# Kernel optimization log

Measured on AMD Instinct MI355X. Metric: run time of the kernel, lower is better.

The kernel has to match this reference:

```python
import jax, jax.numpy as jnp
import numpy as np

STRIDES = (8, 16, 32)
NC = 80            # num_classes
BINS = 16          # dfl_bins
TOPK = 10          # tal_topk
TAL_ALPHA, TAL_BETA = 0.5, 6.0   # ultralytics TaskAlignedAssigner defaults
EPS = 1e-9
FOCAL_A, FOCAL_G = 0.25, 2.0
W_CLS, W_IOU, W_DFL = 0.5, 7.5, 1.5


def _make_grid(H, W, stride):
    ys, xs = jnp.meshgrid(jnp.arange(H, dtype=jnp.float32), jnp.arange(W, dtype=jnp.float32), indexing='ij')
    return jnp.stack([(xs + 0.5) * stride, (ys + 0.5) * stride], -1).reshape(H * W, 2)


def _flatten(p):
    # (B,C,H,W) -> cls (B,N,NC), dfl (B,N,4,BINS); channel layout = [4*BINS dfl | NC cls]
    B, C, H, W = p.shape
    p = p.transpose(0, 2, 3, 1).reshape(B, H * W, C)
    return p[..., 4 * BINS:], p[..., :4 * BINS].reshape(B, H * W, 4, BINS)


def _pairwise_iou(gt, pr):
    # gt (B,G,4), pr (B,N,4) -> iou (B,G,N)
    g = gt[:, :, None]
    p = pr[:, None]
    lt = jnp.maximum(g[..., :2], p[..., :2])
    rb = jnp.minimum(g[..., 2:], p[..., 2:])
    wh = jnp.clip(rb - lt, 0.0)
    inter = wh[..., 0] * wh[..., 1]
    ag = (g[..., 2] - g[..., 0]) * (g[..., 3] - g[..., 1])
    ap = jnp.clip(p[..., 2] - p[..., 0], 0.0) * jnp.clip(p[..., 3] - p[..., 1], 0.0)
    return inter / (ag + ap - inter + EPS)


def _ciou_loss(p, t):
    # elementwise CIoU loss, (...,4) xyxy -> (...)
    px1, py1, px2, py2 = p[..., 0], p[..., 1], p[..., 2], p[..., 3]
    tx1, ty1, tx2, ty2 = t[..., 0], t[..., 1], t[..., 2], t[..., 3]
    w1, h1 = px2 - px1, py2 - py1
    w2, h2 = tx2 - tx1, ty2 - ty1
    inter = jnp.clip(jnp.minimum(px2, tx2) - jnp.maximum(px1, tx1), 0.0) * \
            jnp.clip(jnp.minimum(py2, ty2) - jnp.maximum(py1, ty1), 0.0)
    union = w1 * h1 + w2 * h2 - inter + EPS
    iou = inter / union
    cw = jnp.maximum(px2, tx2) - jnp.minimum(px1, tx1)
    ch = jnp.maximum(py2, ty2) - jnp.minimum(py1, ty1)
    c2 = cw * cw + ch * ch + EPS
    rho2 = ((px1 + px2 - tx1 - tx2) ** 2 + (py1 + py2 - ty1 - ty2) ** 2) / 4.0
    v = (4.0 / np.pi ** 2) * (jnp.arctan(w2 / (h2 + EPS)) - jnp.arctan(w1 / (h1 + EPS))) ** 2
    alpha = jax.lax.stop_gradient(v / (v - iou + (1.0 + EPS)))
    return 1.0 - (iou - rho2 / c2 - v * alpha)


def _tal_assign(cls_prob, pred_boxes, grids, gt_bboxes, gt_labels):
    B, N, C = cls_prob.shape
    G = gt_bboxes.shape[1]
    idx = jnp.broadcast_to(gt_labels[:, None, :], (B, N, G))
    scores = jnp.take_along_axis(cls_prob, idx, axis=2).transpose(0, 2, 1)  # (B,G,N)
    overlaps = _pairwise_iou(gt_bboxes, pred_boxes)                          # (B,G,N)
    align = scores ** TAL_ALPHA * overlaps ** TAL_BETA
    x, y = grids[:, 0], grids[:, 1]
    in_gts = ((x[None, None] > gt_bboxes[..., 0:1]) & (x[None, None] < gt_bboxes[..., 2:3]) &
              (y[None, None] > gt_bboxes[..., 1:2]) & (y[None, None] < gt_bboxes[..., 3:4]))
    metric = jnp.where(in_gts, align, 0.0)
    vals, idxs = jax.lax.top_k(metric, TOPK)                                 # (B,G,TOPK)
    bi = jnp.arange(B)[:, None, None]
    gi = jnp.arange(G)[None, :, None]
    topk_mask = jnp.zeros((B, G, N), bool).at[bi, gi, idxs].set(vals > EPS)
    mask_pos = topk_mask & in_gts
    multi = mask_pos.sum(1) > 1                                              # (B,N)
    is_max = jnp.argmax(overlaps, 1)[:, None, :] == jnp.arange(G)[None, :, None]
    mask_pos = jnp.where(multi[:, None, :], is_max, mask_pos)
    fg = mask_pos.any(1)                                                     # (B,N)
    matched = jnp.argmax(mask_pos, 1)                                        # (B,N)
    mi = jnp.where(fg, matched, -1)
    b2 = jnp.arange(B)[:, None]
    tb = gt_bboxes[b2, matched]                                              # (B,N,4)
    tl = gt_labels[b2, matched]                                              # (B,N)
    mpf = mask_pos.astype(align.dtype)
    align_m = align * mpf
    ov_m = overlaps * mpf
    norm = (align_m * ov_m.max(-1, keepdims=True) / (align_m.max(-1, keepdims=True) + EPS)).max(1)
    ts = jax.nn.one_hot(tl, C, dtype=align.dtype) * norm[..., None] * fg[..., None]
    return ts, tb, fg, mi


def _dfl_targets(gt_bboxes, mi, fgf, grids, stride_map):
    # vectorized version of _make_dfl_targets: soft two-bin scatter per coord
    B, N = mi.shape
    b2 = jnp.arange(B)[:, None]
    boxes = gt_bboxes[b2, jnp.maximum(mi, 0)]                                # (B,N,4)
    cx, cy = grids[:, 0], grids[:, 1]
    d = jnp.stack([jnp.clip(cx - boxes[..., 0], 0.0), jnp.clip(cy - boxes[..., 1], 0.0),
                   jnp.clip(boxes[..., 2] - cx, 0.0), jnp.clip(boxes[..., 3] - cy, 0.0)], -1)
    d = jnp.clip(d / stride_map[None, :, None], 0.0, BINS - 1 - 1e-6)
    lo = jnp.floor(d)
    a = d - lo
    lo_i = lo.astype(jnp.int32)
    up_i = jnp.minimum(lo_i + 1, BINS - 1)
    td = jax.nn.one_hot(lo_i, BINS) * (1.0 - a)[..., None] + jax.nn.one_hot(up_i, BINS) * a[..., None]
    return td * fgf[..., None, None]                                         # (B,N,4,BINS)


def _focal_sum(logits, targets):
    logits = logits.reshape(-1, NC)
    targets = targets.reshape(-1, NC)
    p = jax.nn.sigmoid(logits)
    # stable BCE-with-logits
    ce = jnp.maximum(logits, 0.0) - logits * targets + jnp.log1p(jnp.exp(-jnp.abs(logits)))
    p_t = p * targets + (1.0 - p) * (1.0 - targets)
    a_t = targets * FOCAL_A + (1.0 - targets) * (1.0 - FOCAL_A)
    return (a_t * (1.0 - p_t) ** FOCAL_G * ce).sum()


def _loss(p0, p1, p2, gt_bboxes, gt_labels):
    cls_l, dfl_l, grid_l, str_l = [], [], [], []
    for p, s in zip((p0, p1, p2), STRIDES):
        c, d = _flatten(p)
        cls_l.append(c)
        dfl_l.append(d)
        H, W = p.shape[2], p.shape[3]
        grid_l.append(_make_grid(H, W, s))
        str_l.append(jnp.full((H * W,), float(s), jnp.float32))
    all_cls = jnp.concatenate(cls_l, 1)       # (B,N,NC)
    all_dfl = jnp.concatenate(dfl_l, 1)       # (B,N,4,BINS)
    grids = jnp.concatenate(grid_l, 0)        # (N,2)
    stride_map = jnp.concatenate(str_l, 0)    # (N,)
    # DFL decode: expectation over bins * stride -> ltrb -> xyxy
    dist = (jax.nn.softmax(all_dfl, -1) * jnp.arange(BINS, dtype=jnp.float32)).sum(-1) * stride_map[None, :, None]
    cx, cy = grids[:, 0], grids[:, 1]
    pred_boxes = jnp.stack([cx - dist[..., 0], cy - dist[..., 1], cx + dist[..., 2], cy + dist[..., 3]], -1)
    # assignment under stop_gradient (torch.no_grad in the original)
    cls_prob = jax.lax.stop_gradient(jax.nn.sigmoid(all_cls))
    pb_sg = jax.lax.stop_gradient(pred_boxes)
    ts, tb, fg, mi = _tal_assign(cls_prob, pb_sg, grids, gt_bboxes, gt_labels)
    ts = jax.lax.stop_gradient(ts)
    tb = jax.lax.stop_gradient(tb)
    fgf = fg.astype(jnp.float32)
    den = jnp.maximum(fg.sum(), 1).astype(jnp.float32)
    loss_iou = (_ciou_loss(pred_boxes, tb) * fgf).sum() / den
    tdfl = _dfl_targets(gt_bboxes, mi, fgf, grids, stride_map)
    loss_dfl = -(tdfl * jax.nn.log_softmax(all_dfl, -1)).sum() / den
    loss_cls = _focal_sum(all_cls, ts) / den
    return jnp.stack([W_IOU * loss_iou, W_DFL * loss_dfl, W_CLS * loss_cls])


def setup_inputs() -> dict:
    key = jax.random.key(0)
    ks = jax.random.split(key, 5)
    B, G = 16, 32
    p0 = jax.random.normal(ks[0], (B, 4 * BINS + NC, 80, 80), jnp.float32)
    p1 = jax.random.normal(ks[1], (B, 4 * BINS + NC, 40, 40), jnp.float32)
    p2 = jax.random.normal(ks[2], (B, 4 * BINS + NC, 20, 20), jnp.float32)
    u = jax.random.uniform(ks[3], (B, G, 4), jnp.float32)
    x1 = u[..., 0] * 560.0
    y1 = u[..., 1] * 560.0
    w = u[..., 2] * 140.0 + 20.0
    h = u[..., 3] * 140.0 + 20.0
    gt_bboxes = jnp.stack([x1, y1, jnp.minimum(x1 + w, 640.0), jnp.minimum(y1 + h, 640.0)], -1)
    gt_labels = jax.random.randint(ks[4], (B, G), 0, NC, jnp.int32)
    return {"p0": p0, "p1": p1, "p2": p2, "gt_bboxes": gt_bboxes, "gt_labels": gt_labels}


def reference(p0, p1, p2, gt_bboxes, gt_labels):
    return _loss(p0, p1, p2, gt_bboxes, gt_labels)
```

## Files before the change

### kernel.cpp

```cpp
#include <hip/hip_runtime.h>
#include <hip/hip_bf16.h>
#include <math.h>

#define NCC 80
#define BINS 16
#define NCH 144
#define NB 16
#define NG 32
#define NA 8400
#define HW0 6400
#define HW1 1600
#define HW2 400
#define TOPKK 10
#define EPSF 1e-9f
#define MAXE 13
#define MAXFG (NB*NG*TOPKK)
#define NMASK (NB*NA)
#define FOCAL_BLOCKS 2625

__device__ __forceinline__ void anchor_geom(int n, float& cx, float& cy, float& st){
    if(n < HW0){ int y=n/80, x=n-y*80; st=8.f; cx=(x+0.5f)*8.f; cy=(y+0.5f)*8.f; }
    else if(n < HW0+HW1){ int m=n-HW0; int y=m/40, x=m-y*40; st=16.f; cx=(x+0.5f)*16.f; cy=(y+0.5f)*16.f; }
    else { int m=n-(HW0+HW1); int y=m/20, x=m-y*20; st=32.f; cx=(x+0.5f)*32.f; cy=(y+0.5f)*32.f; }
}

__device__ __forceinline__ const float* level_base(const float* p0, const float* p1, const float* p2,
                                                   int b, int n, int& m, int& hw){
    if(n < HW0){ m=n; hw=HW0; return p0 + (size_t)b*NCH*HW0; }
    if(n < HW0+HW1){ m=n-HW0; hw=HW1; return p1 + (size_t)b*NCH*HW1; }
    m=n-(HW0+HW1); hw=HW2; return p2 + (size_t)b*NCH*HW2;
}

__device__ __forceinline__ float iou_gp(float gx1,float gy1,float gx2,float gy2,
                                        float px1,float py1,float px2,float py2){
    float ltx = fmaxf(gx1, px1), lty = fmaxf(gy1, py1);
    float rbx = fminf(gx2, px2), rby = fminf(gy2, py2);
    float w = fmaxf(rbx-ltx, 0.f), h = fmaxf(rby-lty, 0.f);
    float inter = w*h;
    float ag = (gx2-gx1)*(gy2-gy1);
    float ap = fmaxf(px2-px1,0.f)*fmaxf(py2-py1,0.f);
    return inter/(ag+ap-inter+EPSF);
}

__device__ __forceinline__ float focal0(float x, float& p, float& ce0){
    float ax = fabsf(x);
    float e  = __expf(-ax);
    float r  = 1.f/(1.f+e);
    p   = (x >= 0.f) ? r : 1.f - r;
    ce0 = fmaxf(x,0.f) + __logf(1.f+e);
    return 0.75f*p*p*ce0;
}

__global__ __launch_bounds__(256) void k_decode(const float* __restrict__ p0, const float* __restrict__ p1,
                                                const float* __restrict__ p2, float* __restrict__ boxc,
                                                unsigned* __restrict__ maskg, float* __restrict__ amax,
                                                float* __restrict__ omax, int* __restrict__ cnt){
    int l = blockIdx.x*256 + threadIdx.x;
    if(l < NMASK) maskg[l] = 0u;
    if(l < NB*NG){ amax[l] = 0.f; omax[l] = 0.f; }
    if(l == 0) *cnt = 0;
    int n = l % NA;
    int j = (l / NA) & 3;
    int b = l / (NA*4);
    int m, hw; const float* base = level_base(p0,p1,p2,b,n,m,hw);
    float cx, cy, st; anchor_geom(n,cx,cy,st);
    const float* ch = base + (size_t)(j*BINS)*hw + m;
    float v[BINS]; float mx=-1e30f;
    #pragma unroll
    for(int k=0;k<BINS;k++){ v[k]=ch[(size_t)k*hw]; mx = fmaxf(mx, v[k]); }
    float s=0.f, acc=0.f;
    #pragma unroll
    for(int k=0;k<BINS;k++){ float e=__expf(v[k]-mx); s+=e; acc+=e*(float)k; }
    float d = acc/s*st;
    float out;
    if(j==0) out = cx - d;
    else if(j==1) out = cy - d;
    else if(j==2) out = cx + d;
    else out = cy + d;
    boxc[(size_t)j*NB*NA + (size_t)b*NA + n] = out;
}

__global__ __launch_bounds__(256) void k_assign(const float* __restrict__ p0, const float* __restrict__ p1,
                                                const float* __restrict__ p2, const float* __restrict__ boxc,
                                                const float* __restrict__ gtb, const int* __restrict__ gtl,
                                                unsigned* __restrict__ maskg){
    int wv = threadIdx.x >> 6, lane = threadIdx.x & 63;
    int g = blockIdx.x*4 + wv, b = blockIdx.y;
    const float* gb = gtb + ((size_t)b*NG + g)*4;
    float gx1=gb[0], gy1=gb[1], gx2=gb[2], gy2=gb[3];
    int label = gtl[b*NG+g];
    const float* bx1 = boxc + (size_t)b*NA;
    const float* by1 = bx1 + (size_t)NB*NA;
    const float* bx2 = by1 + (size_t)NB*NA;
    const float* by2 = bx2 + (size_t)NB*NA;

    int xs[3], ys[3], nx[3], cc[3];
    #pragma unroll
    for(int lvl=0; lvl<3; lvl++){
        float s = (float)(8<<lvl); int D = 80>>lvl;
        int x0 = max(0, (int)floorf(gx1/s - 0.5f));
        int x1 = min(D-1, (int)ceilf (gx2/s - 0.5f));
        int y0 = max(0, (int)floorf(gy1/s - 0.5f));
        int y1 = min(D-1, (int)ceilf (gy2/s - 0.5f));
        xs[lvl]=x0; ys[lvl]=y0;
        nx[lvl]=max(0, x1-x0+1);
        int nyv=max(0, y1-y0+1);
        cc[lvl]=nx[lvl]*nyv;
    }
    int t0 = cc[0], t01 = cc[0]+cc[1], total = t01+cc[2];

    float mv[MAXE]; int mn[MAXE];
    #pragma unroll
    for(int j=0;j<MAXE;j++){
        int ci = lane + 64*j;
        float met = -1.f; int n = 0x7fffffff;
        if(ci < total){
            int lvl, rel;
            if(ci < t0){ lvl=0; rel=ci; }
            else if(ci < t01){ lvl=1; rel=ci-t0; }
            else { lvl=2; rel=ci-t01; }
            int yy = ys[lvl] + rel / nx[lvl];
            int xx = xs[lvl] + rel % nx[lvl];
            int D = 80>>lvl; float s = (float)(8<<lvl);
            int off = (lvl==0)?0:((lvl==1)?HW0:(HW0+HW1));
            n = off + yy*D + xx;
            float cx = (xx+0.5f)*s, cy = (yy+0.5f)*s;
            met = 0.f;
            if((cx>gx1)&&(cx<gx2)&&(cy>gy1)&&(cy<gy2)){
                float ov = iou_gp(gx1,gy1,gx2,gy2, bx1[n],by1[n],bx2[n],by2[n]);
                int m,hw; const float* base = level_base(p0,p1,p2,b,n,m,hw);
                float x = base[(size_t)(4*BINS+label)*hw + m];
                float sg = 1.f/(1.f+__expf(-x));
                float ov2 = ov*ov;
                met = sqrtf(sg)*(ov2*ov2*ov2);
            }
        }
        mv[j]=met; mn[j]=n;
    }

    for(int k=0;k<TOPKK;k++){
        float bv = -1.f; int bi = 0x7fffffff;
        #pragma unroll
        for(int j=0;j<MAXE;j++){
            if(mv[j] > bv || (mv[j] == bv && mn[j] < bi)){ bv=mv[j]; bi=mn[j]; }
        }
        #pragma unroll
        for(int off=1; off<64; off<<=1){
            float ov = __shfl_xor(bv, off);
            int   oi = __shfl_xor(bi, off);
            if(ov > bv || (ov == bv && oi < bi)){ bv=ov; bi=oi; }
        }
        if(bv <= EPSF) break;
        bool own = false;
        #pragma unroll
        for(int j=0;j<MAXE;j++){
            if(mn[j] == bi && mv[j] > -1.f){ mv[j] = -1.f; own = true; }
        }
        if(own) atomicOr(&maskg[(size_t)b*NA + bi], 1u<<g);
    }
}

__global__ __launch_bounds__(256) void k_resolve(const float* __restrict__ p0, const float* __restrict__ p1,
                                                 const float* __restrict__ p2, const float* __restrict__ boxc,
                                                 const float* __restrict__ gtb, const int* __restrict__ gtl,
                                                 const unsigned* __restrict__ maskg,
                                                 float* __restrict__ amax, float* __restrict__ omax,
                                                 int* __restrict__ cnt, unsigned* __restrict__ fglist,
                                                 float* __restrict__ fgalign, float* __restrict__ fgx){
    __shared__ float sgt[NG*4];
    __shared__ int wcnt[4];
    __shared__ int sbase;
    int tid = threadIdx.x; int b = blockIdx.y;
    int wv = tid >> 6, lane = tid & 63;
    if(tid < NG*4) sgt[tid] = gtb[(size_t)b*NG*4 + tid];
    __syncthreads();
    int n = blockIdx.x*256 + tid;
    size_t bn = (size_t)b*NA + n;
    unsigned mask = (n < NA) ? maskg[bn] : 0u;
    bool fg = (mask != 0u);

    int match = 0; float ov = 0.f, av = 0.f, x = 0.f;
    if(fg){
        float px1 = boxc[bn], py1 = boxc[(size_t)NB*NA+bn],
              px2 = boxc[2*(size_t)NB*NA+bn], py2 = boxc[3*(size_t)NB*NA+bn];
        if(__popc(mask) > 1){
            float best = -1.f; int bi = 0;
            for(int g=0; g<NG; g++){
                float o = iou_gp(sgt[g*4],sgt[g*4+1],sgt[g*4+2],sgt[g*4+3],px1,py1,px2,py2);
                if(o > best){ best=o; bi=g; }
            }
            match = bi; ov = best;
        } else {
            match = __ffs(mask)-1;
            ov = iou_gp(sgt[match*4],sgt[match*4+1],sgt[match*4+2],sgt[match*4+3],px1,py1,px2,py2);
        }
        int label = gtl[b*NG+match];
        int m,hw; const float* base = level_base(p0,p1,p2,b,n,m,hw);
        x = base[(size_t)(4*BINS+label)*hw + m];
        float sg = 1.f/(1.f+__expf(-x));
        float ov2 = ov*ov;
        av = sqrtf(sg)*(ov2*ov2*ov2);
        atomicMax((int*)&amax[b*NG+match], __float_as_int(av));
        atomicMax((int*)&omax[b*NG+match], __float_as_int(ov));
    }
    unsigned long long bal = __ballot(fg);
    if(lane==0) wcnt[wv] = __popcll(bal);
    __syncthreads();
    if(tid==0){
        int tot = wcnt[0]+wcnt[1]+wcnt[2]+wcnt[3];
        sbase = tot ? atomicAdd(cnt, tot) : 0;
    }
    __syncthreads();
    if(fg){
        int woff = 0;
        for(int w=0; w<wv; w++) woff += wcnt[w];
        int before = __popcll(bal & ((1ull<<lane)-1ull));
        int pos = sbase + woff + before;
        fglist[pos]  = (unsigned)bn | ((unsigned)match << 18);
        fgalign[pos] = av;
        fgx[pos]     = x;
    }
}

__global__ __launch_bounds__(256) void k_fg(const float* __restrict__ p0, const float* __restrict__ p1,
                                            const float* __restrict__ p2, const float* __restrict__ boxc,
                                            const float* __restrict__ gtb, const int* __restrict__ gtl,
                                            const float* __restrict__ amax, const float* __restrict__ omax,
                                            const int* __restrict__ cnt, const unsigned* __restrict__ fglist,
                                            const float* __restrict__ fgalign, const float* __restrict__ fgx,
                                            float* __restrict__ piou, float* __restrict__ pdfl,
                                            float* __restrict__ pfix){
    __shared__ float s4[12];
    int tid = threadIdx.x;
    int i = blockIdx.x*256 + tid;
    float iou_l = 0.f, dfl_l = 0.f, fix_l = 0.f;
    if(i < *cnt){
        unsigned e = fglist[i];
        int bn = e & 0x3FFFF;
        int g  = e >> 18;
        int b  = bn / NA;
        int n  = bn - b*NA;
        float align = fgalign[i];
        float norm = align * omax[b*NG+g] / (amax[b*NG+g] + EPSF);

        const float* gb = gtb + ((size_t)b*NG+g)*4;
        float tx1=gb[0], ty1=gb[1], tx2=gb[2], ty2=gb[3];
        float px1 = boxc[bn], py1 = boxc[(size_t)NB*NA+bn],
              px2 = boxc[2*(size_t)NB*NA+bn], py2 = boxc[3*(size_t)NB*NA+bn];
        float w1=px2-px1, h1=py2-py1, w2=tx2-tx1, h2=ty2-ty1;
        float inter = fmaxf(fminf(px2,tx2)-fmaxf(px1,tx1),0.f) *
                      fmaxf(fminf(py2,ty2)-fmaxf(py1,ty1),0.f);
        float uni = w1*h1 + w2*h2 - inter + EPSF;
        float iou = inter/uni;
        float cwd = fmaxf(px2,tx2)-fminf(px1,tx1);
        float chd = fmaxf(py2,ty2)-fminf(py1,ty1);
        float c2 = cwd*cwd + chd*chd + EPSF;
        float dx = px1+px2-tx1-tx2, dy = py1+py2-ty1-ty2;
        float rho2 = (dx*dx + dy*dy)*0.25f;
        float dv = atanf(w2/(h2+EPSF)) - atanf(w1/(h1+EPSF));
        float v = 0.40528473456935108577f*dv*dv;
        float alpha = v/(v - iou + 1.f + EPSF);
        iou_l = 1.f - (iou - rho2/c2 - v*alpha);
        int m,hw; const float* base = level_base(p0,p1,p2,b,n,m,hw);
        float cx,cy,st; anchor_geom(n,cx,cy,st);
        float dt4[4] = { fmaxf(cx-tx1,0.f), fmaxf(cy-ty1,0.f), fmaxf(tx2-cx,0.f), fmaxf(ty2-cy,0.f) };
        #pragma unroll
        for(int j=0;j<4;j++){
            float d = fminf(fmaxf(dt4[j]/st, 0.f), 14.999999f);
            float lo = floorf(d);
            float a = d - lo;
            int li = (int)lo; int ui = min(li+1, BINS-1);
            float vbuf[BINS]; float mx = -1e30f;
            #pragma unroll
            for(int k=0;k<BINS;k++){ float vv = base[(size_t)(j*BINS+k)*hw + m]; vbuf[k]=vv; mx=fmaxf(mx,vv); }
            float sse = 0.f, xlo = 0.f, xup = 0.f;
            #pragma unroll
            for(int k=0;k<BINS;k++){
                sse += __expf(vbuf[k]-mx);
                if(k==li) xlo = vbuf[k];
                if(k==ui) xup = vbuf[k];
            }
            float lse = mx + __logf(sse);
            dfl_l += -((1.f-a)*(xlo-lse) + a*(xup-lse));
        }
        float fx = fgx[i];
        float p, ce0;
        float f0 = focal0(fx, p, ce0);
        float tv = norm;
        float cet = ce0 - fx*tv;
        float pt = p*tv + (1.f-p)*(1.f-tv);
        float at = 0.25f*tv + 0.75f*(1.f-tv);
        float om = 1.f-pt;
        fix_l = at*om*om*cet - f0;
    }
    #pragma unroll
    for(int off=32; off; off>>=1){
        iou_l += __shfl_down(iou_l, off);
        dfl_l += __shfl_down(dfl_l, off);
        fix_l += __shfl_down(fix_l, off);
    }
    int wv = tid>>6;
    if((tid&63)==0){ s4[wv]=iou_l; s4[4+wv]=dfl_l; s4[8+wv]=fix_l; }
    __syncthreads();
    if(tid==0){
        piou[blockIdx.x] = s4[0]+s4[1]+s4[2]+s4[3];
        pdfl[blockIdx.x] = s4[4]+s4[5]+s4[6]+s4[7];
        pfix[blockIdx.x] = s4[8]+s4[9]+s4[10]+s4[11];
    }
}

__global__ __launch_bounds__(256) void k_focal(const float* __restrict__ p0, const float* __restrict__ p1,
                                               const float* __restrict__ p2, float* __restrict__ pcls){
    __shared__ float s4[4];
    int tid = threadIdx.x;
    int t = blockIdx.x*256 + tid;
    float acc = 0.f;
    #pragma unroll
    for(int it=0; it<4; ++it){
        int i4 = t + it*672000;
        const float4* src;
        if(i4 < 2048000){
            int b = i4 / 128000; int r = i4 - b*128000;
            src = (const float4*)(p0 + (size_t)b*921600 + 409600) + r;
        } else if(i4 < 2560000){
            int j = i4 - 2048000; int b = j / 32000; int r = j - b*32000;
            src = (const float4*)(p1 + (size_t)b*230400 + 102400) + r;
        } else {
            int j = i4 - 2560000; int b = j / 8000; int r = j - b*8000;
            src = (const float4*)(p2 + (size_t)b*57600 + 25600) + r;
        }
        float4 x4 = *src;
        float p, c;
        acc += focal0(x4.x, p, c);
        acc += focal0(x4.y, p, c);
        acc += focal0(x4.z, p, c);
        acc += focal0(x4.w, p, c);
    }
    #pragma unroll
    for(int off=32; off; off>>=1) acc += __shfl_down(acc, off);
    if((tid&63)==0) s4[tid>>6] = acc;
    __syncthreads();
    if(tid==0) pcls[blockIdx.x] = s4[0]+s4[1]+s4[2]+s4[3];
}

__global__ __launch_bounds__(256) void k_final(const float* __restrict__ pcls, const float* __restrict__ piou,
                                               const float* __restrict__ pdfl, const float* __restrict__ pfix,
                                               const int* __restrict__ cnt, float* __restrict__ out){
    __shared__ float sa[4], sb[4], sc[4], sd[4];
    int tid = threadIdx.x;
    float a = 0.f;
    for(int i=tid; i<FOCAL_BLOCKS; i+=256) a += pcls[i];
    float b3=0.f, c3=0.f, d3=0.f;
    if(tid < MAXFG/256){ b3=piou[tid]; c3=pdfl[tid]; d3=pfix[tid]; }
    #pragma unroll
    for(int off=32; off; off>>=1){
        a  += __shfl_down(a,  off);
        b3 += __shfl_down(b3, off);
        c3 += __shfl_down(c3, off);
        d3 += __shfl_down(d3, off);
    }
    if((tid&63)==0){ int w=tid>>6; sa[w]=a; sb[w]=b3; sc[w]=c3; sd[w]=d3; }
    __syncthreads();
    if(tid==0){
        float A=sa[0]+sa[1]+sa[2]+sa[3], B=sb[0]+sb[1]+sb[2]+sb[3];
        float C=sc[0]+sc[1]+sc[2]+sc[3], D=sd[0]+sd[1]+sd[2]+sd[3];
        int c = *cnt;
        float den = (float)(c > 1 ? c : 1);
        out[0] = 7.5f * B / den;
        out[1] = 1.5f * C / den;
        out[2] = 0.5f * (A + D) / den;
    }
}

extern "C" void kernel_launch(void* const* d_in, const int* in_sizes, int n_in,
                              void* d_out, int out_size, void* d_ws, size_t ws_size,
                              hipStream_t stream) {
    (void)in_sizes; (void)n_in; (void)out_size; (void)ws_size;
    const float* p0  = (const float*)d_in[0];
    const float* p1  = (const float*)d_in[1];
    const float* p2  = (const float*)d_in[2];
    const float* gtb = (const float*)d_in[3];
    const int*   gtl = (const int*)d_in[4];
    float* out = (float*)d_out;

    char* ws = (char*)d_ws;
    const size_t COMP = (size_t)NB*NA*4;
    size_t off = 0;
    int*      cnt    = (int*)     (ws + off); off += 16;
    float*    amax   = (float*)   (ws + off); off += NB*NG*4;
    float*    omax   = (float*)   (ws + off); off += NB*NG*4;
    unsigned* maskg  = (unsigned*)(ws + off); off += COMP;
    float*    boxc   = (float*)   (ws + off); off += 4*COMP;
    unsigned* fglist = (unsigned*)(ws + off); off += MAXFG*4;
    float*    fgalign= (float*)   (ws + off); off += MAXFG*4;
    float*    fgx    = (float*)   (ws + off); off += MAXFG*4;
    float*    pcls   = (float*)   (ws + off); off += FOCAL_BLOCKS*4;
    float*    piou   = (float*)   (ws + off); off += (MAXFG/256)*4;
    float*    pdfl   = (float*)   (ws + off); off += (MAXFG/256)*4;
    float*    pfix   = (float*)   (ws + off); off += (MAXFG/256)*4;

    dim3 blk(256);
    k_decode <<<2100,              blk, 0, stream>>>(p0,p1,p2, boxc, maskg, amax, omax, cnt);
    k_assign <<<dim3(NG/4,NB),     blk, 0, stream>>>(p0,p1,p2, boxc, gtb, gtl, maskg);
    k_resolve<<<dim3(33,NB),       blk, 0, stream>>>(p0,p1,p2, boxc, gtb, gtl, maskg,
                                                     amax, omax, cnt, fglist, fgalign, fgx);
    k_fg     <<<MAXFG/256,         blk, 0, stream>>>(p0,p1,p2, boxc, gtb, gtl, amax, omax,
                                                     cnt, fglist, fgalign, fgx, piou, pdfl, pfix);
    k_focal  <<<FOCAL_BLOCKS,      blk, 0, stream>>>(p0,p1,p2, pcls);
    k_final  <<<1,                 blk, 0, stream>>>(pcls, piou, pdfl, pfix, cnt, out);
}
```

Before: 160.1 us.

## Vectorize box decode, use block-per-GT assignment and wave-per-foreground losses

Box decode now processes four adjacent anchors per thread with float4 loads and stores, cutting the thread count. TAL assignment gives each GT a full 256-thread block, storing candidate metrics in shared memory and doing a block-wide top-k reduction, instead of one wave per GT holding everything in registers. The foreground loss kernel maps one wave per foreground item, computing the DFL log-softmax with 16-lane shuffles across lanes. This trades fewer serial loops per thread for extra block syncs in the top-k loop and more blocks overall.

```diff
diff --git a/kernel.cpp b/kernel.cpp
--- a/kernel.cpp
+++ b/kernel.cpp
@@ -13,8 +13,9 @@
 #define HW2 400
 #define TOPKK 10
 #define EPSF 1e-9f
-#define MAXE 13
+#define MAXC 832
 #define MAXFG (NB*NG*TOPKK)
+#define FGB (MAXFG/4)
 #define NMASK (NB*NA)
 #define FOCAL_BLOCKS 2625
 
@@ -56,36 +57,55 @@
                                                 unsigned* __restrict__ maskg, float* __restrict__ amax,
                                                 float* __restrict__ omax, int* __restrict__ cnt){
     int l = blockIdx.x*256 + threadIdx.x;
-    if(l < NMASK) maskg[l] = 0u;
+    maskg[l] = 0u;
     if(l < NB*NG){ amax[l] = 0.f; omax[l] = 0.f; }
     if(l == 0) *cnt = 0;
-    int n = l % NA;
-    int j = (l / NA) & 3;
-    int b = l / (NA*4);
-    int m, hw; const float* base = level_base(p0,p1,p2,b,n,m,hw);
-    float cx, cy, st; anchor_geom(n,cx,cy,st);
-    const float* ch = base + (size_t)(j*BINS)*hw + m;
-    float v[BINS]; float mx=-1e30f;
-    #pragma unroll
-    for(int k=0;k<BINS;k++){ v[k]=ch[(size_t)k*hw]; mx = fmaxf(mx, v[k]); }
-    float s=0.f, acc=0.f;
-    #pragma unroll
-    for(int k=0;k<BINS;k++){ float e=__expf(v[k]-mx); s+=e; acc+=e*(float)k; }
-    float d = acc/s*st;
-    float out;
-    if(j==0) out = cx - d;
-    else if(j==1) out = cy - d;
-    else if(j==2) out = cx + d;
-    else out = cy + d;
-    boxc[(size_t)j*NB*NA + (size_t)b*NA + n] = out;
+    int q = l % 2100;
+    int j = (l / 2100) & 3;
+    int b = l / 8400;
+    const float* pl; int hw, m, n0, D; float st;
+    if(q < 1600){ pl=p0; hw=HW0; m=4*q;        n0=m;         D=80; st=8.f; }
+    else if(q < 2000){ pl=p1; hw=HW1; m=4*(q-1600); n0=HW0+m;     D=40; st=16.f; }
+    else { pl=p2; hw=HW2; m=4*(q-2000); n0=HW0+HW1+m; D=20; st=32.f; }
+    const float* ch = pl + ((size_t)b*NCH + j*BINS)*hw + m;
+    float4 v[BINS];
+    float4 mx = make_float4(-1e30f,-1e30f,-1e30f,-1e30f);
+    #pragma unroll
+    for(int k=0;k<BINS;k++){
+        v[k] = *(const float4*)(ch + (size_t)k*hw);
+        mx.x=fmaxf(mx.x,v[k].x); mx.y=fmaxf(mx.y,v[k].y);
+        mx.z=fmaxf(mx.z,v[k].z); mx.w=fmaxf(mx.w,v[k].w);
+    }
+    float4 s = make_float4(0,0,0,0), acc = make_float4(0,0,0,0);
+    #pragma unroll
+    for(int k=0;k<BINS;k++){
+        float fk=(float)k; float e;
+        e=__expf(v[k].x-mx.x); s.x+=e; acc.x+=e*fk;
+        e=__expf(v[k].y-mx.y); s.y+=e; acc.y+=e*fk;
+        e=__expf(v[k].z-mx.z); s.z+=e; acc.z+=e*fk;
+        e=__expf(v[k].w-mx.w); s.w+=e; acc.w+=e*fk;
+    }
+    float4 d = make_float4(acc.x/s.x*st, acc.y/s.y*st, acc.z/s.z*st, acc.w/s.w*st);
+    int row = m / D, col = m - row*D;
+    float cy = (row+0.5f)*st;
+    float cx0=(col+0.5f)*st, cx1=(col+1.5f)*st, cx2=(col+2.5f)*st, cx3=(col+3.5f)*st;
+    float4 o;
+    if(j==0)      o = make_float4(cx0-d.x, cx1-d.y, cx2-d.z, cx3-d.w);
+    else if(j==1) o = make_float4(cy -d.x, cy -d.y, cy -d.z, cy -d.w);
+    else if(j==2) o = make_float4(cx0+d.x, cx1+d.y, cx2+d.z, cx3+d.w);
+    else          o = make_float4(cy +d.x, cy +d.y, cy +d.z, cy +d.w);
+    *(float4*)(boxc + (size_t)j*NB*NA + (size_t)b*NA + n0) = o;
 }
 
 __global__ __launch_bounds__(256) void k_assign(const float* __restrict__ p0, const float* __restrict__ p1,
                                                 const float* __restrict__ p2, const float* __restrict__ boxc,
                                                 const float* __restrict__ gtb, const int* __restrict__ gtl,
                                                 unsigned* __restrict__ maskg){
-    int wv = threadIdx.x >> 6, lane = threadIdx.x & 63;
-    int g = blockIdx.x*4 + wv, b = blockIdx.y;
+    __shared__ float metric[MAXC];
+    __shared__ int   candn[MAXC];
+    __shared__ float rv[4]; __shared__ int ri[4];
+    __shared__ float sbest; __shared__ int sbidx;
+    int g = blockIdx.x, b = blockIdx.y, tid = threadIdx.x;
     const float* gb = gtb + ((size_t)b*NG + g)*4;
     float gx1=gb[0], gy1=gb[1], gx2=gb[2], gy2=gb[3];
     int label = gtl[b*NG+g];
@@ -94,7 +114,7 @@
     const float* bx2 = by1 + (size_t)NB*NA;
     const float* by2 = bx2 + (size_t)NB*NA;
 
-    int xs[3], ys[3], nx[3], cc[3];
+    int xs[3], ys[3], nxv[3], cc[3];
     #pragma unroll
     for(int lvl=0; lvl<3; lvl++){
         float s = (float)(8<<lvl); int D = 80>>lvl;
@@ -103,60 +123,63 @@
         int y0 = max(0, (int)floorf(gy1/s - 0.5f));
         int y1 = min(D-1, (int)ceilf (gy2/s - 0.5f));
         xs[lvl]=x0; ys[lvl]=y0;
-        nx[lvl]=max(0, x1-x0+1);
+        nxv[lvl]=max(0, x1-x0+1);
         int nyv=max(0, y1-y0+1);
-        cc[lvl]=nx[lvl]*nyv;
+        cc[lvl]=nxv[lvl]*nyv;
     }
     int t0 = cc[0], t01 = cc[0]+cc[1], total = t01+cc[2];
 
-    float mv[MAXE]; int mn[MAXE];
-    #pragma unroll
-    for(int j=0;j<MAXE;j++){
-        int ci = lane + 64*j;
-        float met = -1.f; int n = 0x7fffffff;
-        if(ci < total){
-            int lvl, rel;
-            if(ci < t0){ lvl=0; rel=ci; }
-            else if(ci < t01){ lvl=1; rel=ci-t0; }
-            else { lvl=2; rel=ci-t01; }
-            int yy = ys[lvl] + rel / nx[lvl];
-            int xx = xs[lvl] + rel % nx[lvl];
-            int D = 80>>lvl; float s = (float)(8<<lvl);
-            int off = (lvl==0)?0:((lvl==1)?HW0:(HW0+HW1));
-            n = off + yy*D + xx;
-            float cx = (xx+0.5f)*s, cy = (yy+0.5f)*s;
-            met = 0.f;
-            if((cx>gx1)&&(cx<gx2)&&(cy>gy1)&&(cy<gy2)){
-                float ov = iou_gp(gx1,gy1,gx2,gy2, bx1[n],by1[n],bx2[n],by2[n]);
-                int m,hw; const float* base = level_base(p0,p1,p2,b,n,m,hw);
-                float x = base[(size_t)(4*BINS+label)*hw + m];
-                float sg = 1.f/(1.f+__expf(-x));
-                float ov2 = ov*ov;
-                met = sqrtf(sg)*(ov2*ov2*ov2);
-            }
-        }
-        mv[j]=met; mn[j]=n;
-    }
+    for(int c=tid; c<total; c+=256){
+        int lvl, rel;
+        if(c < t0){ lvl=0; rel=c; }
+        else if(c < t01){ lvl=1; rel=c-t0; }
+        else { lvl=2; rel=c-t01; }
+        int yy = ys[lvl] + rel / nxv[lvl];
+        int xx = xs[lvl] + rel % nxv[lvl];
+        int D = 80>>lvl; float s = (float)(8<<lvl);
+        int off = (lvl==0)?0:((lvl==1)?HW0:(HW0+HW1));
+        int n = off + yy*D + xx;
+        float cx = (xx+0.5f)*s, cy = (yy+0.5f)*s;
+        float met = 0.f;
+        if((cx>gx1)&&(cx<gx2)&&(cy>gy1)&&(cy<gy2)){
+            float ov = iou_gp(gx1,gy1,gx2,gy2, bx1[n],by1[n],bx2[n],by2[n]);
+            int m,hw; const float* base = level_base(p0,p1,p2,b,n,m,hw);
+            float x = base[(size_t)(4*BINS+label)*hw + m];
+            float sg = 1.f/(1.f+__expf(-x));
+            float o2 = ov*ov;
+            met = sqrtf(sg)*(o2*o2*o2);
+        }
+        metric[c] = met; candn[c] = n;
+    }
+    __syncthreads();
 
     for(int k=0;k<TOPKK;k++){
         float bv = -1.f; int bi = 0x7fffffff;
+        for(int c=tid; c<total; c+=256){
+            float v = metric[c];
+            if(v > bv){ bv=v; bi=c; }
+        }
         #pragma unroll
-        for(int j=0;j<MAXE;j++){
-            if(mv[j] > bv || (mv[j] == bv && mn[j] < bi)){ bv=mv[j]; bi=mn[j]; }
-        }
-        #pragma unroll
-        for(int off=1; off<64; off<<=1){
-            float ov = __shfl_xor(bv, off);
-            int   oi = __shfl_xor(bi, off);
+        for(int o=1; o<64; o<<=1){
+            float ov = __shfl_xor(bv, o);
+            int   oi = __shfl_xor(bi, o);
             if(ov > bv || (ov == bv && oi < bi)){ bv=ov; bi=oi; }
         }
-        if(bv <= EPSF) break;
-        bool own = false;
-        #pragma unroll
-        for(int j=0;j<MAXE;j++){
-            if(mn[j] == bi && mv[j] > -1.f){ mv[j] = -1.f; own = true; }
-        }
-        if(own) atomicOr(&maskg[(size_t)b*NA + bi], 1u<<g);
+        if((tid&63)==0){ rv[tid>>6]=bv; ri[tid>>6]=bi; }
+        __syncthreads();
+        if(tid==0){
+            float fb=rv[0]; int fi=ri[0];
+            #pragma unroll
+            for(int w=1; w<4; w++)
+                if(rv[w]>fb || (rv[w]==fb && ri[w]<fi)){ fb=rv[w]; fi=ri[w]; }
+            sbest = fb; sbidx = fi;
+            if(fb > EPSF){
+                metric[fi] = -1.f;
+                atomicOr(&maskg[(size_t)b*NA + candn[fi]], 1u<<g);
+            }
+        }
+        __syncthreads();
+        if(sbest <= EPSF) break;
     }
 }
 
@@ -224,15 +247,15 @@
 
 __global__ __launch_bounds__(256) void k_fg(const float* __restrict__ p0, const float* __restrict__ p1,
                                             const float* __restrict__ p2, const float* __restrict__ boxc,
-                                            const float* __restrict__ gtb, const int* __restrict__ gtl,
+                                            const float* __restrict__ gtb,
                                             const float* __restrict__ amax, const float* __restrict__ omax,
                                             const int* __restrict__ cnt, const unsigned* __restrict__ fglist,
                                             const float* __restrict__ fgalign, const float* __restrict__ fgx,
                                             float* __restrict__ piou, float* __restrict__ pdfl,
                                             float* __restrict__ pfix){
     __shared__ float s4[12];
-    int tid = threadIdx.x;
-    int i = blockIdx.x*256 + tid;
+    int tid = threadIdx.x, wv = tid>>6, lane = tid&63;
+    int i = blockIdx.x*4 + wv;
     float iou_l = 0.f, dfl_l = 0.f, fix_l = 0.f;
     if(i < *cnt){
         unsigned e = fglist[i];
@@ -242,65 +265,61 @@
         int n  = bn - b*NA;
         float align = fgalign[i];
         float norm = align * omax[b*NG+g] / (amax[b*NG+g] + EPSF);
-
         const float* gb = gtb + ((size_t)b*NG+g)*4;
         float tx1=gb[0], ty1=gb[1], tx2=gb[2], ty2=gb[3];
         float px1 = boxc[bn], py1 = boxc[(size_t)NB*NA+bn],
               px2 = boxc[2*(size_t)NB*NA+bn], py2 = boxc[3*(size_t)NB*NA+bn];
-        float w1=px2-px1, h1=py2-py1, w2=tx2-tx1, h2=ty2-ty1;
-        float inter = fmaxf(fminf(px2,tx2)-fmaxf(px1,tx1),0.f) *
-                      fmaxf(fminf(py2,ty2)-fmaxf(py1,ty1),0.f);
-        float uni = w1*h1 + w2*h2 - inter + EPSF;
-        float iou = inter/uni;
-        float cwd = fmaxf(px2,tx2)-fminf(px1,tx1);
-        float chd = fmaxf(py2,ty2)-fminf(py1,ty1);
-        float c2 = cwd*cwd + chd*chd + EPSF;
-        float dx = px1+px2-tx1-tx2, dy = py1+py2-ty1-ty2;
-        float rho2 = (dx*dx + dy*dy)*0.25f;
-        float dv = atanf(w2/(h2+EPSF)) - atanf(w1/(h1+EPSF));
-        float v = 0.40528473456935108577f*dv*dv;
-        float alpha = v/(v - iou + 1.f + EPSF);
-        iou_l = 1.f - (iou - rho2/c2 - v*alpha);
         int m,hw; const float* base = level_base(p0,p1,p2,b,n,m,hw);
         float cx,cy,st; anchor_geom(n,cx,cy,st);
-        float dt4[4] = { fmaxf(cx-tx1,0.f), fmaxf(cy-ty1,0.f), fmaxf(tx2-cx,0.f), fmaxf(ty2-cy,0.f) };
+        int j = lane>>4, k = lane&15;
+        float x = base[(size_t)lane*hw + m];
+        float dt = (j==0)?(cx-tx1):((j==1)?(cy-ty1):((j==2)?(tx2-cx):(ty2-cy)));
+        float d = fminf(fmaxf(dt,0.f)/st, 14.999999f);
+        float lo = floorf(d); float a = d-lo;
+        int li = (int)lo; int ui = min(li+1, BINS-1);
+        float mx = x;
         #pragma unroll
-        for(int j=0;j<4;j++){
-            float d = fminf(fmaxf(dt4[j]/st, 0.f), 14.999999f);
-            float lo = floorf(d);
-            float a = d - lo;
-            int li = (int)lo; int ui = min(li+1, BINS-1);
-            float vbuf[BINS]; float mx = -1e30f;
-            #pragma unroll
-            for(int k=0;k<BINS;k++){ float vv = base[(size_t)(j*BINS+k)*hw + m]; vbuf[k]=vv; mx=fmaxf(mx,vv); }
-            float sse = 0.f, xlo = 0.f, xup = 0.f;
-            #pragma unroll
-            for(int k=0;k<BINS;k++){
-                sse += __expf(vbuf[k]-mx);
-                if(k==li) xlo = vbuf[k];
-                if(k==ui) xup = vbuf[k];
-            }
-            float lse = mx + __logf(sse);
-            dfl_l += -((1.f-a)*(xlo-lse) + a*(xup-lse));
-        }
-        float fx = fgx[i];
-        float p, ce0;
-        float f0 = focal0(fx, p, ce0);
-        float tv = norm;
-        float cet = ce0 - fx*tv;
-        float pt = p*tv + (1.f-p)*(1.f-tv);
-        float at = 0.25f*tv + 0.75f*(1.f-tv);
-        float om = 1.f-pt;
-        fix_l = at*om*om*cet - f0;
-    }
-    #pragma unroll
-    for(int off=32; off; off>>=1){
-        iou_l += __shfl_down(iou_l, off);
-        dfl_l += __shfl_down(dfl_l, off);
-        fix_l += __shfl_down(fix_l, off);
-    }
-    int wv = tid>>6;
-    if((tid&63)==0){ s4[wv]=iou_l; s4[4+wv]=dfl_l; s4[8+wv]=fix_l; }
+        for(int o=1;o<16;o<<=1) mx = fmaxf(mx, __shfl_xor(mx,o));
+        float ex = __expf(x-mx);
+        float se = ex;
+        #pragma unroll
+        for(int o=1;o<16;o<<=1) se += __shfl_xor(se,o);
+        float lse = mx + __logf(se);
+        float coef = ((k==li)?(1.f-a):0.f) + ((k==ui)?a:0.f);
+        dfl_l = -coef*(x-lse);
+        if(lane==0){
+            float w1=px2-px1, h1=py2-py1, w2=tx2-tx1, h2=ty2-ty1;
+            float inter = fmaxf(fminf(px2,tx2)-fmaxf(px1,tx1),0.f) *
+                          fmaxf(fminf(py2,ty2)-fmaxf(py1,ty1),0.f);
+            float uni = w1*h1 + w2*h2 - inter + EPSF;
+            float iou = inter/uni;
+            float cwd = fmaxf(px2,tx2)-fminf(px1,tx1);
+            float chd = fmaxf(py2,ty2)-fminf(py1,ty1);
+            float c2 = cwd*cwd + chd*chd + EPSF;
+            float dx = px1+px2-tx1-tx2, dy = py1+py2-ty1-ty2;
+            float rho2 = (dx*dx + dy*dy)*0.25f;
+            float dv = atanf(w2/(h2+EPSF)) - atanf(w1/(h1+EPSF));
+            float v = 0.40528473456935108577f*dv*dv;
+            float alpha = v/(v - iou + 1.f + EPSF);
+            iou_l = 1.f - (iou - rho2/c2 - v*alpha);
+            float fx = fgx[i];
+            float p, ce0;
+            float f0 = focal0(fx, p, ce0);
+            float tv = norm;
+            float cet = ce0 - fx*tv;
+            float pt = p*tv + (1.f-p)*(1.f-tv);
+            float at = 0.25f*tv + 0.75f*(1.f-tv);
+            float om = 1.f-pt;
+            fix_l = at*om*om*cet - f0;
+        }
+    }
+    #pragma unroll
+    for(int o=32; o; o>>=1){
+        iou_l += __shfl_down(iou_l, o);
+        dfl_l += __shfl_down(dfl_l, o);
+        fix_l += __shfl_down(fix_l, o);
+    }
+    if(lane==0){ s4[wv]=iou_l; s4[4+wv]=dfl_l; s4[8+wv]=fix_l; }
     __syncthreads();
     if(tid==0){
         piou[blockIdx.x] = s4[0]+s4[1]+s4[2]+s4[3];
@@ -348,10 +367,9 @@
                                                const int* __restrict__ cnt, float* __restrict__ out){
     __shared__ float sa[4], sb[4], sc[4], sd[4];
     int tid = threadIdx.x;
-    float a = 0.f;
+    float a = 0.f, b3 = 0.f, c3 = 0.f, d3 = 0.f;
     for(int i=tid; i<FOCAL_BLOCKS; i+=256) a += pcls[i];
-    float b3=0.f, c3=0.f, d3=0.f;
-    if(tid < MAXFG/256){ b3=piou[tid]; c3=pdfl[tid]; d3=pfix[tid]; }
+    for(int i=tid; i<FGB; i+=256){ b3 += piou[i]; c3 += pdfl[i]; d3 += pfix[i]; }
     #pragma unroll
     for(int off=32; off; off>>=1){
         a  += __shfl_down(a,  off);
@@ -395,17 +413,17 @@
     float*    fgalign= (float*)   (ws + off); off += MAXFG*4;
     float*    fgx    = (float*)   (ws + off); off += MAXFG*4;
     float*    pcls   = (float*)   (ws + off); off += FOCAL_BLOCKS*4;
-    float*    piou   = (float*)   (ws + off); off += (MAXFG/256)*4;
-    float*    pdfl   = (float*)   (ws + off); off += (MAXFG/256)*4;
-    float*    pfix   = (float*)   (ws + off); off += (MAXFG/256)*4;
+    float*    piou   = (float*)   (ws + off); off += FGB*4;
+    float*    pdfl   = (float*)   (ws + off); off += FGB*4;
+    float*    pfix   = (float*)   (ws + off); off += FGB*4;
 
     dim3 blk(256);
-    k_decode <<<2100,              blk, 0, stream>>>(p0,p1,p2, boxc, maskg, amax, omax, cnt);
-    k_assign <<<dim3(NG/4,NB),     blk, 0, stream>>>(p0,p1,p2, boxc, gtb, gtl, maskg);
-    k_resolve<<<dim3(33,NB),       blk, 0, stream>>>(p0,p1,p2, boxc, gtb, gtl, maskg,
-                                                     amax, omax, cnt, fglist, fgalign, fgx);
-    k_fg     <<<MAXFG/256,         blk, 0, stream>>>(p0,p1,p2, boxc, gtb, gtl, amax, omax,
-                                                     cnt, fglist, fgalign, fgx, piou, pdfl, pfix);
-    k_focal  <<<FOCAL_BLOCKS,      blk, 0, stream>>>(p0,p1,p2, pcls);
-    k_final  <<<1,                 blk, 0, stream>>>(pcls, piou, pdfl, pfix, cnt, out);
-}
+    k_decode <<<525,             blk, 0, stream>>>(p0,p1,p2, boxc, maskg, amax, omax, cnt);
+    k_assign <<<dim3(NG,NB),     blk, 0, stream>>>(p0,p1,p2, boxc, gtb, gtl, maskg);
+    k_resolve<<<dim3(33,NB),     blk, 0, stream>>>(p0,p1,p2, boxc, gtb, gtl, maskg,
+                                                   amax, omax, cnt, fglist, fgalign, fgx);
+    k_fg     <<<FGB,             blk, 0, stream>>>(p0,p1,p2, boxc, gtb, amax, omax,
+                                                   cnt, fglist, fgalign, fgx, piou, pdfl, pfix);
+    k_focal  <<<FOCAL_BLOCKS,    blk, 0, stream>>>(p0,p1,p2, pcls);
+    k_final  <<<1,               blk, 0, stream>>>(pcls, piou, pdfl, pfix, cnt, out);
+}
```

Result: faster. 151.6 us (-5.3%).
